# Kernel tuning notes

Measured on AMD Instinct MI355X. Metric: run time of the kernel, lower is better.

Reference implementation:

```python
import jax, jax.numpy as jnp
import numpy as np

TOPK, NPRO, NALP, NADS = 9, 31, 24, 37
EPS = 1e-9


def _pairwise_iou(b1, b2, eps=1e-6):
    # b1: (M,4) xyxy, b2: (N,4) xyxy -> (M,N)
    a1 = (b1[:, 2] - b1[:, 0]) * (b1[:, 3] - b1[:, 1])
    a2 = (b2[:, 2] - b2[:, 0]) * (b2[:, 3] - b2[:, 1])
    lt = jnp.maximum(b1[:, None, :2], b2[None, :, :2])
    rb = jnp.minimum(b1[:, None, 2:], b2[None, :, 2:])
    wh = jnp.clip(rb - lt, 0.0)
    ov = wh[..., 0] * wh[..., 1]
    union = jnp.maximum(a1[:, None] + a2[None, :] - ov, eps)
    return ov / union


def _dist_calculator(gt, anc):
    # center-to-center euclidean distance; returns (M,N) dists and (N,2) anchor centers
    gt_pts = jnp.stack([(gt[:, 0] + gt[:, 2]) / 2, (gt[:, 1] + gt[:, 3]) / 2], -1)
    ac_pts = jnp.stack([(anc[:, 0] + anc[:, 2]) / 2, (anc[:, 1] + anc[:, 3]) / 2], -1)
    d = jnp.sqrt(((gt_pts[:, None, :] - ac_pts[None, :, :]) ** 2).sum(-1))
    return d, ac_pts


def _batched_iou(b1, b2, eps=EPS):
    # b1 (b,M,4), b2 (b,N,4) -> (b,M,N)
    p1, p2 = b1[:, :, None, :2], b1[:, :, None, 2:]
    g1, g2 = b2[:, None, :, :2], b2[:, None, :, 2:]
    wh = jnp.clip(jnp.minimum(p2, g2) - jnp.maximum(p1, g1), 0.0)
    ov = wh[..., 0] * wh[..., 1]
    a1 = jnp.clip(p2 - p1, 0.0).prod(-1)
    a2 = jnp.clip(g2 - g1, 0.0).prod(-1)
    return ov / (a1 + a2 - ov + eps)


def setup_inputs() -> dict:
    key = jax.random.key(0)
    k = jax.random.split(key, 8)
    strides, img = (8, 16, 32), 1280
    anchors, levels = [], []
    for s in strides:
        n = img // s
        c = (jnp.arange(n, dtype=jnp.float32) + 0.5) * s
        cy, cx = jnp.meshgrid(c, c, indexing="ij")
        cx, cy = cx.reshape(-1), cy.reshape(-1)
        h = 2.5 * s  # cell anchor half-size = 5*stride/2 (YOLOv6 ATSS convention)
        anchors.append(jnp.stack([cx - h, cy - h, cx + h, cy + h], -1))
        levels.append(n * n)
    anc_bboxes = jnp.concatenate(anchors, 0)  # (33600, 4)
    bs, n_max = 8, 64
    cxy = jax.random.uniform(k[0], (bs, n_max, 2), minval=100.0, maxval=1180.0)
    wh = jax.random.uniform(k[1], (bs, n_max, 2), minval=20.0, maxval=300.0)
    gt_bboxes = jnp.concatenate([cxy - wh / 2, cxy + wh / 2], -1)
    x1, y1, x2, y2 = (gt_bboxes[..., i] for i in range(4))
    gt_corners = jnp.stack([x1, y1, x2, y1, x2, y2, x1, y2], -1)
    gt_pro = jax.random.randint(k[2], (bs, n_max, 1), 0, NPRO).astype(jnp.float32)
    gt_alp = jax.random.randint(k[3], (bs, n_max, 1), 0, NALP).astype(jnp.float32)
    gt_ads = jax.random.randint(k[4], (bs, n_max, 6), 0, NADS).astype(jnp.float32)
    n_valid = jax.random.randint(k[5], (bs, 1), 8, n_max + 1)
    mask_gt = (jnp.arange(n_max)[None, :] < n_valid).astype(jnp.float32)[..., None]
    pd_bboxes = anc_bboxes[None] + jax.random.normal(k[6], (bs, anc_bboxes.shape[0], 4)) * 8.0
    return {"anc_bboxes": anc_bboxes, "n_level_bboxes": levels, "gt_pro": gt_pro,
            "gt_alp": gt_alp, "gt_ads": gt_ads, "gt_bboxes": gt_bboxes,
            "gt_corners": gt_corners, "mask_gt": mask_gt, "pd_bboxes": pd_bboxes}


def reference(anc_bboxes, n_level_bboxes, gt_pro, gt_alp, gt_ads, gt_bboxes, gt_corners, mask_gt, pd_bboxes):
    bs, n_max, _ = gt_bboxes.shape
    n_anchors = anc_bboxes.shape[0]
    overlaps = _pairwise_iou(gt_bboxes.reshape(-1, 4), anc_bboxes).reshape(bs, n_max, n_anchors)
    distances, ac_points = _dist_calculator(gt_bboxes.reshape(-1, 4), anc_bboxes)
    distances = distances.reshape(bs, n_max, n_anchors)

    # --- per-level topk candidate selection ---
    mgt = mask_gt[..., 0] > 0
    b_idx = jnp.arange(bs)[:, None, None]
    g_idx = jnp.arange(n_max)[None, :, None]
    iic, cidx, start = [], [], 0
    for L in [int(v) for v in n_level_bboxes]:
        d = distances[..., start:start + L]
        k = min(TOPK, L)
        _, idxs = jax.lax.top_k(-d, k)  # smallest-distance anchors, (b,M,k)
        cidx.append(idxs + start)
        idxs_m = jnp.where(mgt[..., None], idxs, 0)
        cnt = jnp.zeros((bs, n_max, L), distances.dtype).at[b_idx, g_idx, idxs_m].add(1.0)
        iic.append(jnp.where(cnt > 1, jnp.zeros_like(cnt), cnt))
        start += L
    is_in_candidate = jnp.concatenate(iic, -1)      # (b,M,N)
    candidate_idxs = jnp.concatenate(cidx, -1)      # (b,M,K)

    # --- threshold = mean + std of candidate IoUs per gt ---
    cand_ov = jnp.where(is_in_candidate > 0, overlaps, jnp.zeros_like(overlaps))
    co = jnp.take_along_axis(cand_ov, candidate_idxs, axis=-1)  # (b,M,K)
    thr = co.mean(-1, keepdims=True) + jnp.std(co, axis=-1, ddof=1, keepdims=True)
    is_pos = jnp.where(cand_ov > thr, is_in_candidate, jnp.zeros_like(is_in_candidate))

    # --- anchor centers inside gt boxes ---
    lt = ac_points[None, None, :, :] - gt_bboxes[:, :, None, :2]
    rb = gt_bboxes[:, :, None, 2:] - ac_points[None, None, :, :]
    is_in_gts = (jnp.concatenate([lt, rb], -1).min(-1) > EPS).astype(distances.dtype)
    mask_pos = is_pos * is_in_gts * mask_gt  # (b,M,N)

    # --- resolve anchors claimed by multiple gts via max overlap ---
    fg = mask_pos.sum(-2)
    multi = fg[:, None, :] > 1
    is_max = jax.nn.one_hot(overlaps.argmax(1), n_max, dtype=mask_pos.dtype).transpose(0, 2, 1)
    mask_pos = jnp.where(multi, is_max, mask_pos)
    fg_mask = mask_pos.sum(-2)                 # (b,N)
    target_gt_idx = mask_pos.argmax(-2)        # (b,N)

    # --- gather targets ---
    fgb = fg_mask > 0
    target_pro = jnp.where(fgb, jnp.take_along_axis(gt_pro[..., 0], target_gt_idx, 1), NPRO).astype(jnp.int32)
    target_alp = jnp.where(fgb, jnp.take_along_axis(gt_alp[..., 0], target_gt_idx, 1), NALP).astype(jnp.int32)
    target_ad0_5 = [jnp.where(fgb, jnp.take_along_axis(gt_ads[..., i], target_gt_idx, 1), NADS).astype(jnp.int32)
                    for i in range(6)]
    target_bboxes = jnp.take_along_axis(gt_bboxes, target_gt_idx[..., None], 1)
    target_corners = jnp.take_along_axis(gt_corners, target_gt_idx[..., None], 1)
    pro_scores = jax.nn.one_hot(target_pro, NPRO + 1, dtype=jnp.float32)[..., :NPRO]
    alp_scores = jax.nn.one_hot(target_alp, NALP + 1, dtype=jnp.float32)[..., :NALP]
    ads_scores = [jax.nn.one_hot(t, NADS + 1, dtype=jnp.float32)[..., :NADS] for t in target_ad0_5]

    # --- rescale scores by best pred-vs-gt IoU among assigned pairs ---
    ious = (_batched_iou(gt_bboxes, pd_bboxes) * mask_pos).max(-2)[..., None]  # (b,N,1)
    pro_scores = pro_scores * ious
    alp_scores = alp_scores * ious
    ads_scores = [s * ious for s in ads_scores]

    return (target_pro, target_alp, *target_ad0_5, target_bboxes, target_corners,
            pro_scores, alp_scores, *ads_scores, fgb)
```

## Files before the change

### kernel.cpp

```cpp
#include <hip/hip_runtime.h>
#include <hip/hip_bf16.h>

#pragma clang fp contract(off)

#define NB 8
#define NG 64
#define NA 33600
#define KTOP 9
#define NCAND 27
#define NPRO 31
#define NALP 24
#define NADS 37

__device__ __forceinline__ float pair_iou(float x1, float y1, float x2, float y2,
                                          float ax1, float ay1, float ax2, float ay2) {
    float a1 = (x2 - x1) * (y2 - y1);
    float a2 = (ax2 - ax1) * (ay2 - ay1);
    float w = fminf(x2, ax2) - fmaxf(x1, ax1); w = fmaxf(w, 0.0f);
    float h = fminf(y2, ay2) - fmaxf(y1, ay1); h = fmaxf(h, 0.0f);
    float ov = w * h;
    float un = a1 + a2 - ov; un = fmaxf(un, 1e-6f);
    return ov / un;
}

__global__ __launch_bounds__(256) void k_cand(
    const float* __restrict__ anc,
    const float* __restrict__ gt,
    const float* __restrict__ mgt,
    unsigned long long* __restrict__ gbits)
{
    int bg = blockIdx.x;
    int b = bg >> 6;
    int g = bg & 63;
    if (mgt[bg] <= 0.0f) return;

    const float x1 = gt[bg * 4 + 0], y1 = gt[bg * 4 + 1];
    const float x2 = gt[bg * 4 + 2], y2 = gt[bg * 4 + 3];
    const float gx = (x1 + x2) * 0.5f, gy = (y1 + y2) * 0.5f;

    __shared__ float sd[256][KTOP];
    __shared__ int   si[256][KTOP];
    __shared__ int   cand[NCAND];

    const int tid = threadIdx.x;
    const int starts[3] = {0, 25600, 32000};
    const int lens[3]   = {25600, 6400, 1600};

    for (int lev = 0; lev < 3; ++lev) {
        float d9[KTOP]; int i9[KTOP];
        #pragma unroll
        for (int j = 0; j < KTOP; ++j) { d9[j] = INFINITY; i9[j] = 0x7fffffff; }

        const int s = starts[lev], L = lens[lev];
        for (int li = tid; li < L; li += 256) {
            int a = s + li;
            float ax = (anc[a * 4 + 0] + anc[a * 4 + 2]) * 0.5f;
            float ay = (anc[a * 4 + 1] + anc[a * 4 + 3]) * 0.5f;
            float dx = gx - ax, dy = gy - ay;
            float d = sqrtf(dx * dx + dy * dy);
            if (d < d9[KTOP - 1] || (d == d9[KTOP - 1] && li < i9[KTOP - 1])) {
                int j = KTOP - 1;
                while (j > 0 && (d < d9[j - 1] || (d == d9[j - 1] && li < i9[j - 1]))) {
                    d9[j] = d9[j - 1]; i9[j] = i9[j - 1]; --j;
                }
                d9[j] = d; i9[j] = li;
            }
        }

        for (int off = 128; off >= 1; off >>= 1) {
            #pragma unroll
            for (int j = 0; j < KTOP; ++j) { sd[tid][j] = d9[j]; si[tid][j] = i9[j]; }
            __syncthreads();
            if (tid < off) {
                float md[KTOP]; int mi[KTOP];
                int p = 0, q = 0;
                #pragma unroll
                for (int j = 0; j < KTOP; ++j) {
                    float da = d9[p];            int ia = i9[p];
                    float db = sd[tid + off][q]; int ib = si[tid + off][q];
                    bool takeA = (da < db) || (da == db && ia <= ib);
                    if (takeA) { md[j] = da; mi[j] = ia; ++p; }
                    else       { md[j] = db; mi[j] = ib; ++q; }
                }
                #pragma unroll
                for (int j = 0; j < KTOP; ++j) { d9[j] = md[j]; i9[j] = mi[j]; }
            }
            __syncthreads();
        }
        if (tid == 0) {
            #pragma unroll
            for (int j = 0; j < KTOP; ++j) cand[lev * KTOP + j] = s + i9[j];
        }
        __syncthreads();
    }

    if (tid == 0) {
        float co[NCAND];
        float sum = 0.0f;
        for (int j = 0; j < NCAND; ++j) {
            int a = cand[j];
            co[j] = pair_iou(x1, y1, x2, y2,
                             anc[a * 4 + 0], anc[a * 4 + 1], anc[a * 4 + 2], anc[a * 4 + 3]);
            sum += co[j];
        }
        float m = sum / 27.0f;
        float v = 0.0f;
        for (int j = 0; j < NCAND; ++j) { float dd = co[j] - m; v += dd * dd; }
        float thr = m + sqrtf(v / 26.0f);
        for (int j = 0; j < NCAND; ++j) {
            if (co[j] > thr) {
                int a = cand[j];
                float ax = (anc[a * 4 + 0] + anc[a * 4 + 2]) * 0.5f;
                float ay = (anc[a * 4 + 1] + anc[a * 4 + 3]) * 0.5f;
                float mn = fminf(fminf(ax - x1, ay - y1), fminf(x2 - ax, y2 - ay));
                if (mn > 1e-9f) {
                    atomicOr(&gbits[(unsigned long long)b * NA + a], 1ull << g);
                }
            }
        }
    }
}

__global__ __launch_bounds__(256) void k_assign(
    const float* __restrict__ anc,
    const float* __restrict__ gt_pro,
    const float* __restrict__ gt_alp,
    const float* __restrict__ gt_ads,
    const float* __restrict__ gt,
    const float* __restrict__ gt_cn,
    const float* __restrict__ pd,
    const unsigned long long* __restrict__ gbits,
    float* __restrict__ out)
{
    const int t = blockIdx.x * 256 + threadIdx.x;
    if (t >= NB * NA) return;
    const int b = t / NA;
    const int a = t - b * NA;

    unsigned long long m = gbits[t];
    int fg = __popcll(m);
    if (fg > 1) {
        float ax1 = anc[a * 4 + 0], ay1 = anc[a * 4 + 1];
        float ax2 = anc[a * 4 + 2], ay2 = anc[a * 4 + 3];
        float aarea = (ax2 - ax1) * (ay2 - ay1);
        float best = -INFINITY; int bgi = 0;
        for (int g = 0; g < NG; ++g) {
            const float* G = gt + ((size_t)b * NG + g) * 4;
            float gx1 = G[0], gy1 = G[1], gx2 = G[2], gy2 = G[3];
            float a1 = (gx2 - gx1) * (gy2 - gy1);
            float w = fminf(gx2, ax2) - fmaxf(gx1, ax1); w = fmaxf(w, 0.0f);
            float h = fminf(gy2, ay2) - fmaxf(gy1, ay1); h = fmaxf(h, 0.0f);
            float ov = w * h;
            float un = a1 + aarea - ov; un = fmaxf(un, 1e-6f);
            float iou = ov / un;
            if (iou > best) { best = iou; bgi = g; }
        }
        m = 1ull << bgi;
    }
    const bool fgb = (m != 0ull);
    const int tg = fgb ? (__ffsll((unsigned long long)m) - 1) : 0;

    const size_t row = (size_t)b * NG + tg;
    const float bx1 = gt[row * 4 + 0], by1 = gt[row * 4 + 1];
    const float bx2 = gt[row * 4 + 2], by2 = gt[row * 4 + 3];
    const float pro = gt_pro[row];
    const float alp = gt_alp[row];

    float iou_pd = 0.0f;
    if (fgb) {
        const float* P = pd + ((size_t)b * NA + a) * 4;
        float px1 = P[0], py1 = P[1], px2 = P[2], py2 = P[3];
        float w = fminf(bx2, px2) - fmaxf(bx1, px1); w = fmaxf(w, 0.0f);
        float h = fminf(by2, py2) - fmaxf(by1, py1); h = fmaxf(h, 0.0f);
        float ov = w * h;
        float a1 = fmaxf(bx2 - bx1, 0.0f) * fmaxf(by2 - by1, 0.0f);
        float a2 = fmaxf(px2 - px1, 0.0f) * fmaxf(py2 - py1, 0.0f);
        iou_pd = ov / (a1 + a2 - ov + 1e-9f);
    }

    const size_t S0 = (size_t)NB * NA;

    out[t] = fgb ? pro : (float)NPRO;
    out[S0 + t] = fgb ? alp : (float)NALP;
    float adsv[6];
    #pragma unroll
    for (int i = 0; i < 6; ++i) {
        adsv[i] = gt_ads[row * 6 + i];
        out[S0 * (2 + i) + t] = fgb ? adsv[i] : (float)NADS;
    }
    {
        float* ob = out + S0 * 8 + (size_t)t * 4;
        ob[0] = bx1; ob[1] = by1; ob[2] = bx2; ob[3] = by2;
    }
    {
        float* oc = out + S0 * 12 + (size_t)t * 8;
        #pragma unroll
        for (int i = 0; i < 8; ++i) oc[i] = gt_cn[row * 8 + i];
    }
    if (fgb) {
        out[S0 * 20 + (size_t)t * NPRO + (int)pro] = iou_pd;
        out[S0 * 20 + S0 * NPRO + (size_t)t * NALP + (int)alp] = iou_pd;
        const size_t ads_base = S0 * 20 + S0 * NPRO + S0 * NALP;
        #pragma unroll
        for (int i = 0; i < 6; ++i) {
            out[ads_base + (size_t)i * S0 * NADS + (size_t)t * NADS + (int)adsv[i]] = iou_pd;
        }
    }
    out[S0 * 20 + S0 * NPRO + S0 * NALP + (size_t)6 * S0 * NADS + t] = fgb ? 1.0f : 0.0f;
}

extern "C" void kernel_launch(void* const* d_in, const int* in_sizes, int n_in,
                              void* d_out, int out_size, void* d_ws, size_t ws_size,
                              hipStream_t stream) {
    const float* anc    = (const float*)d_in[0];
    const float* gt_pro = (const float*)d_in[2];
    const float* gt_alp = (const float*)d_in[3];
    const float* gt_ads = (const float*)d_in[4];
    const float* gt_bb  = (const float*)d_in[5];
    const float* gt_cn  = (const float*)d_in[6];
    const float* mgt    = (const float*)d_in[7];
    const float* pd     = (const float*)d_in[8];

    unsigned long long* gbits = (unsigned long long*)d_ws;
    float* out = (float*)d_out;

    hipMemsetAsync(d_ws, 0, (size_t)NB * NA * sizeof(unsigned long long), stream);
    hipMemsetAsync(d_out, 0, (size_t)out_size * sizeof(float), stream);

    hipLaunchKernelGGL(k_cand, dim3(NB * NG), dim3(256), 0, stream,
                       anc, gt_bb, mgt, gbits);
    hipLaunchKernelGGL(k_assign, dim3((NB * NA) / 256), dim3(256), 0, stream,
                       anc, gt_pro, gt_alp, gt_ads, gt_bb, gt_cn, pd, gbits, out);
}
```

Measured before the change: 499.7 us.

## Replace full output memset with dense score-writing kernel and vectorized stores

Drops the memset of the whole output buffer. k_assign now records per-anchor packed class indices and the fg IoU in workspace, and a new k_scores kernel writes every element of the one-hot score tensors with float4 stores, so the roughly 300 MB output is written once instead of zeroed and then scatter-written. The box and corner copies now use float4 loads and stores, and the gbits memset becomes a small zeroing kernel. This adds an extra kernel launch and some workspace traffic, and k_scores does an integer divide per element.

Result: slower. 521.5 us (+4.4%).

```diff
diff --git a/kernel.cpp b/kernel.cpp
--- a/kernel.cpp
+++ b/kernel.cpp
@@ -11,6 +11,7 @@
 #define NPRO 31
 #define NALP 24
 #define NADS 37
+#define S0 268800
 
 __device__ __forceinline__ float pair_iou(float x1, float y1, float x2, float y2,
                                           float ax1, float ay1, float ax2, float ay2) {
@@ -21,6 +22,11 @@
     float ov = w * h;
     float un = a1 + a2 - ov; un = fmaxf(un, 1e-6f);
     return ov / un;
+}
+
+__global__ __launch_bounds__(256) void k_zero_gbits(unsigned long long* __restrict__ g) {
+    int t = blockIdx.x * 256 + threadIdx.x;
+    if (t < S0) g[t] = 0ull;
 }
 
 __global__ __launch_bounds__(256) void k_cand(
@@ -130,16 +136,17 @@
     const float* __restrict__ gt_cn,
     const float* __restrict__ pd,
     const unsigned long long* __restrict__ gbits,
+    float* __restrict__ iou_fg,
+    unsigned long long* __restrict__ cls8,
     float* __restrict__ out)
 {
     const int t = blockIdx.x * 256 + threadIdx.x;
-    if (t >= NB * NA) return;
+    if (t >= S0) return;
     const int b = t / NA;
     const int a = t - b * NA;
 
     unsigned long long m = gbits[t];
-    int fg = __popcll(m);
-    if (fg > 1) {
+    if (__popcll(m) > 1) {
         float ax1 = anc[a * 4 + 0], ay1 = anc[a * 4 + 1];
         float ax2 = anc[a * 4 + 2], ay2 = anc[a * 4 + 3];
         float aarea = (ax2 - ax1) * (ay2 - ay1);
@@ -161,8 +168,8 @@
     const int tg = fgb ? (__ffsll((unsigned long long)m) - 1) : 0;
 
     const size_t row = (size_t)b * NG + tg;
-    const float bx1 = gt[row * 4 + 0], by1 = gt[row * 4 + 1];
-    const float bx2 = gt[row * 4 + 2], by2 = gt[row * 4 + 3];
+    const float4 gbox = *(const float4*)(gt + row * 4);
+    const float bx1 = gbox.x, by1 = gbox.y, bx2 = gbox.z, by2 = gbox.w;
     const float pro = gt_pro[row];
     const float alp = gt_alp[row];
 
@@ -178,35 +185,71 @@
         iou_pd = ov / (a1 + a2 - ov + 1e-9f);
     }
 
-    const size_t S0 = (size_t)NB * NA;
-
-    out[t] = fgb ? pro : (float)NPRO;
-    out[S0 + t] = fgb ? alp : (float)NALP;
-    float adsv[6];
+    out[t]       = fgb ? pro : (float)NPRO;
+    out[S0 + t]  = fgb ? alp : (float)NALP;
+    unsigned long long packed = ((unsigned long long)(unsigned)(int)pro) |
+                                (((unsigned long long)(unsigned)(int)alp) << 8);
     #pragma unroll
     for (int i = 0; i < 6; ++i) {
-        adsv[i] = gt_ads[row * 6 + i];
-        out[S0 * (2 + i) + t] = fgb ? adsv[i] : (float)NADS;
-    }
+        float av = gt_ads[row * 6 + i];
+        out[(size_t)S0 * (2 + i) + t] = fgb ? av : (float)NADS;
+        packed |= ((unsigned long long)(unsigned)(int)av) << (8 * (2 + i));
+    }
+    *(float4*)(out + (size_t)S0 * 8 + (size_t)t * 4) = gbox;
     {
-        float* ob = out + S0 * 8 + (size_t)t * 4;
-        ob[0] = bx1; ob[1] = by1; ob[2] = bx2; ob[3] = by2;
-    }
-    {
-        float* oc = out + S0 * 12 + (size_t)t * 8;
-        #pragma unroll
-        for (int i = 0; i < 8; ++i) oc[i] = gt_cn[row * 8 + i];
-    }
-    if (fgb) {
-        out[S0 * 20 + (size_t)t * NPRO + (int)pro] = iou_pd;
-        out[S0 * 20 + S0 * NPRO + (size_t)t * NALP + (int)alp] = iou_pd;
-        const size_t ads_base = S0 * 20 + S0 * NPRO + S0 * NALP;
-        #pragma unroll
-        for (int i = 0; i < 6; ++i) {
-            out[ads_base + (size_t)i * S0 * NADS + (size_t)t * NADS + (int)adsv[i]] = iou_pd;
-        }
-    }
-    out[S0 * 20 + S0 * NPRO + S0 * NALP + (size_t)6 * S0 * NADS + t] = fgb ? 1.0f : 0.0f;
+        const float4* cn = (const float4*)(gt_cn + row * 8);
+        float4* oc = (float4*)(out + (size_t)S0 * 12 + (size_t)t * 8);
+        oc[0] = cn[0]; oc[1] = cn[1];
+    }
+    out[(size_t)S0 * 297 + t] = fgb ? 1.0f : 0.0f;
+
+    iou_fg[t] = fgb ? iou_pd : 0.0f;
+    cls8[t] = packed;
+}
+
+template <int NC>
+__device__ __forceinline__ float4 score4(size_t fin,
+                                         const unsigned long long* __restrict__ cls8,
+                                         const float* __restrict__ iouv,
+                                         int byteIdx) {
+    unsigned t = (unsigned)(fin / NC);
+    unsigned c = (unsigned)(fin - (size_t)t * NC);
+    float4 v;
+    float* pv = &v.x;
+    unsigned tj = t, cj = c;
+    #pragma unroll
+    for (int j = 0; j < 4; ++j) {
+        unsigned cls = (unsigned)((cls8[tj] >> (8 * byteIdx)) & 0xFFull);
+        pv[j] = (cj == cls) ? iouv[tj] : 0.0f;
+        ++cj; if (cj == NC) { cj = 0; ++tj; }
+    }
+    return v;
+}
+
+__global__ __launch_bounds__(256) void k_scores(
+    const unsigned long long* __restrict__ cls8,
+    const float* __restrict__ iouv,
+    float* __restrict__ score)
+{
+    const size_t TOT4 = (size_t)S0 * 277 / 4;
+    size_t idx = (size_t)blockIdx.x * 256 + threadIdx.x;
+    if (idx >= TOT4) return;
+    size_t f = idx * 4;
+    const size_t PRO_END = (size_t)S0 * NPRO;
+    const size_t ALP_END = PRO_END + (size_t)S0 * NALP;
+    const size_t ADS_SZ  = (size_t)S0 * NADS;
+    float4 v;
+    if (f < PRO_END) {
+        v = score4<NPRO>(f, cls8, iouv, 0);
+    } else if (f < ALP_END) {
+        v = score4<NALP>(f - PRO_END, cls8, iouv, 1);
+    } else {
+        size_t r = f - ALP_END;
+        int p = (int)(r / ADS_SZ);
+        size_t rp = r - (size_t)p * ADS_SZ;
+        v = score4<NADS>(rp, cls8, iouv, 2 + p);
+    }
+    *(float4*)(score + f) = v;
 }
 
 extern "C" void kernel_launch(void* const* d_in, const int* in_sizes, int n_in,
@@ -221,14 +264,19 @@
     const float* mgt    = (const float*)d_in[7];
     const float* pd     = (const float*)d_in[8];
 
-    unsigned long long* gbits = (unsigned long long*)d_ws;
+    char* ws = (char*)d_ws;
+    unsigned long long* gbits = (unsigned long long*)ws;
+    float* iou_fg             = (float*)(ws + (size_t)S0 * 8);
+    unsigned long long* cls8  = (unsigned long long*)(ws + (size_t)S0 * 12);
     float* out = (float*)d_out;
 
-    hipMemsetAsync(d_ws, 0, (size_t)NB * NA * sizeof(unsigned long long), stream);
-    hipMemsetAsync(d_out, 0, (size_t)out_size * sizeof(float), stream);
-
+    hipLaunchKernelGGL(k_zero_gbits, dim3((S0 + 255) / 256), dim3(256), 0, stream, gbits);
     hipLaunchKernelGGL(k_cand, dim3(NB * NG), dim3(256), 0, stream,
                        anc, gt_bb, mgt, gbits);
-    hipLaunchKernelGGL(k_assign, dim3((NB * NA) / 256), dim3(256), 0, stream,
-                       anc, gt_pro, gt_alp, gt_ads, gt_bb, gt_cn, pd, gbits, out);
-}
+    hipLaunchKernelGGL(k_assign, dim3((S0 + 255) / 256), dim3(256), 0, stream,
+                       anc, gt_pro, gt_alp, gt_ads, gt_bb, gt_cn, pd, gbits,
+                       iou_fg, cls8, out);
+    const size_t TOT4 = (size_t)S0 * 277 / 4;
+    hipLaunchKernelGGL(k_scores, dim3((unsigned)((TOT4 + 255) / 256)), dim3(256), 0, stream,
+                       cls8, iou_fg, out + (size_t)S0 * 20);
+}
```
